# Kernel tuning notes

Measured on AMD Instinct MI355X. Metric: run time of the kernel, lower is better.

## Reference

```python
import jax, jax.numpy as jnp
from jax import lax
import numpy as np

EMBED = 20
FILTERS = 16
KSIZES = (1, 3, 5, 7, 9)
LIN_IN = 7 * len(KSIZES) * FILTERS  # 560
LIN_DIM = 64
SEQ_LENS = {'pep': 12, 'a1': 7, 'a2': 8, 'a3': 16, 'b1': 6, 'b2': 7, 'b3': 18}
BATCH = 16384


def setup_inputs() -> dict:
    key = jax.random.key(0)
    keys = jax.random.split(key, 16)
    inp = {}
    for i, (name, L) in enumerate(SEQ_LENS.items()):
        inp[name] = jax.random.normal(keys[i], (BATCH, EMBED, L), dtype=jnp.float32)
    # Conv weights: one stacked array per kernel size, [7 sequences, FILTERS, EMBED, k]
    for j, k in enumerate(KSIZES):
        inp[f'Wk{k}'] = jax.random.normal(keys[7 + j], (7, FILTERS, EMBED, k), dtype=jnp.float32) * 0.1
    inp['lin1_w'] = jax.random.normal(keys[12], (LIN_DIM, LIN_IN), dtype=jnp.float32) * 0.05
    inp['lin1_b'] = jnp.zeros((LIN_DIM,), dtype=jnp.float32)
    inp['lin2_w'] = jax.random.normal(keys[13], (1, LIN_DIM), dtype=jnp.float32) * 0.1
    inp['lin2_b'] = jnp.zeros((1,), dtype=jnp.float32)
    return inp


def _conv_relu_gmax(x, w):
    # x: [B, C, L], w: [F, C, k] -> SAME conv + ReLU + global max over length -> [B, F]
    y = lax.conv_general_dilated(x, w, window_strides=(1,), padding='SAME',
                                 dimension_numbers=('NCH', 'OIH', 'NCH'))
    return jnp.max(jax.nn.relu(y), axis=-1)


def _branch(x, ws):
    # x scaled by 1/5 as in the torch forward; concat pooled features over kernel sizes
    x = x / 5.0
    return jnp.concatenate([_conv_relu_gmax(x, w) for w in ws], axis=1)  # [B, 5*F]


def reference(pep, a1, a2, a3, b1, b2, b3, Wk1, Wk3, Wk5, Wk7, Wk9,
              lin1_w, lin1_b, lin2_w, lin2_b):
    seqs = [pep, a1, a2, a3, b1, b2, b3]
    Wks = [Wk1, Wk3, Wk5, Wk7, Wk9]
    feats = jnp.concatenate(
        [_branch(seqs[i], [W[i] for W in Wks]) for i in range(7)], axis=1)  # [B, 560]
    # Dropout is identity at inference.
    h = jax.nn.sigmoid(feats @ lin1_w.T + lin1_b)  # [B, 64]
    out = h @ lin2_w.T + lin2_b                    # [B, 1]
    return out.reshape(-1)                          # [B]
```

## Files before the change

kernel.cpp:

```cpp
#include <hip/hip_runtime.h>
#include <stdint.h>
#include <stddef.h>

typedef short bfrag __attribute__((ext_vector_type(8)));
typedef float f32x4 __attribute__((ext_vector_type(4)));

#define NSEQ 7

__constant__ int c_ks[5] = {1, 3, 5, 7, 9};

#define SLO0 3
#define SLO1 2
#define SLO2 1
#define SLO3 0
#define SLO4 0
#define SN0 1
#define SN1 3
#define SN2 5
#define SN3 6
#define SN4 7

static __device__ __forceinline__ unsigned short f2bf(float f) {
  unsigned int u = __float_as_uint(f);
  u += 0x7FFFu + ((u >> 16) & 1u);
  return (unsigned short)(u >> 16);
}

struct PrepArgs {
  const float* Wk[5];
  const float* lin1_w;
  bfrag* Wpack;
  bfrag* lin1pack;
};

__global__ __launch_bounds__(256) void prep_kernel(PrepArgs a) {
  int tid = blockIdx.x * 256 + threadIdx.x;
  const int NW = NSEQ * 5 * 7 * 64;
  if (tid < NW) {
    int lane = tid & 63, rest = tid >> 6;
    int step = rest % 7, nt = (rest / 7) % 5, seq = rest / 35;
    int quad = lane >> 4, f = lane & 15;
    int ks = c_ks[nt], off = (9 - ks) >> 1;
    const float* W = a.Wk[nt];
    bfrag s;
#pragma unroll
    for (int j = 0; j < 8; ++j) {
      int k = step * 32 + quad * 8 + j;
      int t = k / 24, c = k % 24;
      int tap = t - off;
      float val = 0.f;
      if (c < 20 && tap >= 0 && tap < ks)
        val = W[((seq * 16 + f) * 20 + c) * ks + tap] * 0.2f;
      s[j] = (short)f2bf(val);
    }
    a.Wpack[tid] = s;
  } else if (tid < NW + 4 * 18 * 64) {
    int t2 = tid - NW;
    int lane = t2 & 63, rest = t2 >> 6;
    int step = rest % 18, nt = rest / 18;
    int quad = lane >> 4, col = lane & 15;
    int n = nt * 16 + col;
    bfrag s;
#pragma unroll
    for (int j = 0; j < 8; ++j) {
      int k = step * 32 + quad * 8 + j;
      float val = (k < 560) ? a.lin1_w[n * 560 + k] : 0.f;
      s[j] = (short)f2bf(val);
    }
    a.lin1pack[t2] = s;
  }
}

struct ConvArgs {
  const float* x[NSEQ];
  const bfrag* Wpack;
  unsigned short* feats;
};

static __device__ __forceinline__ void store_feat(unsigned short* feats, int b, int k, float v) {
  int step = k >> 5, q = (k >> 3) & 3, j = k & 7;
  feats[((size_t)(b >> 4) * 18 + step) * 512 + (q * 16 + (b & 15)) * 8 + j] = f2bf(v);
}

template <int Lc, int SHIFTc, int MTc, int TBBv, int Pv>
__device__ __forceinline__ void conv_body(unsigned short* xl, const ConvArgs& a,
                                          const int seq, const int b0) {
  const int tid = threadIdx.x;
  const float* xg = a.x[seq];

  for (int i = tid; i < TBBv * Pv * 24 / 8; i += 256) ((uint4*)xl)[i] = uint4{0, 0, 0, 0};
  __syncthreads();
  {
    constexpr int NF4 = TBBv * 20 * Lc / 4;
    const float* xb = xg + (size_t)b0 * 20 * Lc;
    for (int i4 = tid; i4 < NF4; i4 += 256) {
      float4 v = *(const float4*)(xb + i4 * 4);
#pragma unroll
      for (int e = 0; e < 4; ++e) {
        int flat = i4 * 4 + e;
        int b = flat / (20 * Lc), rem = flat % (20 * Lc);
        int c = rem / Lc, xi = rem % Lc;
        float val = (e == 0) ? v.x : (e == 1) ? v.y : (e == 2) ? v.z : v.w;
        xl[(b * Pv + 4 + xi) * 24 + c] = f2bf(val);
      }
    }
  }
  __syncthreads();

  const int wave = tid >> 6, lane = tid & 63, quad = lane >> 4, m = lane & 15;

  const bfrag* wp = a.Wpack + (size_t)(seq * 5 * 7) * 64 + lane;
  bfrag Bf[22];
  {
    int bi = 0;
#pragma unroll
    for (int i = 0; i < SN0; ++i) Bf[bi++] = wp[(0 * 7 + SLO0 + i) * 64];
#pragma unroll
    for (int i = 0; i < SN1; ++i) Bf[bi++] = wp[(1 * 7 + SLO1 + i) * 64];
#pragma unroll
    for (int i = 0; i < SN2; ++i) Bf[bi++] = wp[(2 * 7 + SLO2 + i) * 64];
#pragma unroll
    for (int i = 0; i < SN3; ++i) Bf[bi++] = wp[(3 * 7 + SLO3 + i) * 64];
#pragma unroll
    for (int i = 0; i < SN4; ++i) Bf[bi++] = wp[(4 * 7 + SLO4 + i) * 64];
  }

  constexpr int njobs = (MTc == 2) ? TBBv : ((TBBv << SHIFTc) >> 4);
  constexpr int bpt = (MTc == 1 && SHIFTc == 3) ? 2 : 1;
  constexpr int lmask = (1 << SHIFTc) - 1;

  for (int job = wave; job < njobs; job += 4) {
    float v0 = 0.f, v1 = 0.f, v2 = 0.f, v3 = 0.f, v4 = 0.f;
#pragma unroll
    for (int sub = 0; sub < MTc; ++sub) {
      int bl, l;
      if (MTc == 2) { bl = job; l = sub * 2 + m; }
      else { int r = job * 16 + m; bl = r >> SHIFTc; l = r & lmask; }
      const unsigned short* arow = &xl[(bl * Pv + l) * 24 + quad * 8];
      f32x4 acc0 = {0.f, 0.f, 0.f, 0.f}, acc1 = acc0, acc2 = acc0, acc3 = acc0, acc4 = acc0;
#pragma unroll
      for (int s = 0; s < 7; ++s) {
        bfrag Af = *(const bfrag*)(arow + s * 32);
        if (s >= SLO0 && s < SLO0 + SN0)
          acc0 = __builtin_amdgcn_mfma_f32_16x16x32_bf16(Af, Bf[0 + s - SLO0], acc0, 0, 0, 0);
        if (s >= SLO1 && s < SLO1 + SN1)
          acc1 = __builtin_amdgcn_mfma_f32_16x16x32_bf16(Af, Bf[1 + s - SLO1], acc1, 0, 0, 0);
        if (s >= SLO2 && s < SLO2 + SN2)
          acc2 = __builtin_amdgcn_mfma_f32_16x16x32_bf16(Af, Bf[4 + s - SLO2], acc2, 0, 0, 0);
        if (s >= SLO3 && s < SLO3 + SN3)
          acc3 = __builtin_amdgcn_mfma_f32_16x16x32_bf16(Af, Bf[9 + s - SLO3], acc3, 0, 0, 0);
        acc4 = __builtin_amdgcn_mfma_f32_16x16x32_bf16(Af, Bf[15 + s], acc4, 0, 0, 0);
      }
#pragma unroll
      for (int r4 = 0; r4 < 4; ++r4) {
        bool ok = (MTc == 2) ? true : (((quad * 4 + r4) & lmask) < Lc);
        v0 = fmaxf(v0, ok ? acc0[r4] : 0.f);
        v1 = fmaxf(v1, ok ? acc1[r4] : 0.f);
        v2 = fmaxf(v2, ok ? acc2[r4] : 0.f);
        v3 = fmaxf(v3, ok ? acc3[r4] : 0.f);
        v4 = fmaxf(v4, ok ? acc4[r4] : 0.f);
      }
    }
    v0 = fmaxf(v0, __shfl_xor(v0, 16));
    v1 = fmaxf(v1, __shfl_xor(v1, 16));
    v2 = fmaxf(v2, __shfl_xor(v2, 16));
    v3 = fmaxf(v3, __shfl_xor(v3, 16));
    v4 = fmaxf(v4, __shfl_xor(v4, 16));
    if (bpt == 1) {
      v0 = fmaxf(v0, __shfl_xor(v0, 32));
      v1 = fmaxf(v1, __shfl_xor(v1, 32));
      v2 = fmaxf(v2, __shfl_xor(v2, 32));
      v3 = fmaxf(v3, __shfl_xor(v3, 32));
      v4 = fmaxf(v4, __shfl_xor(v4, 32));
      if (lane < 16) {
        int b = b0 + job, kb = seq * 80 + lane;
        store_feat(a.feats, b, kb, v0);      store_feat(a.feats, b, kb + 16, v1);
        store_feat(a.feats, b, kb + 32, v2); store_feat(a.feats, b, kb + 48, v3);
        store_feat(a.feats, b, kb + 64, v4);
      }
    } else {
      if ((lane & 16) == 0) {
        int b = b0 + job * 2 + (lane >> 5), kb = seq * 80 + (lane & 15);
        store_feat(a.feats, b, kb, v0);      store_feat(a.feats, b, kb + 16, v1);
        store_feat(a.feats, b, kb + 32, v2); store_feat(a.feats, b, kb + 48, v3);
        store_feat(a.feats, b, kb + 64, v4);
      }
    }
  }
}

__global__ __launch_bounds__(256, 4) void conv_kernel(ConvArgs a) {
  __shared__ __align__(16) unsigned short xl[32 * 25 * 24];
  const int bid = blockIdx.x;
  if (bid < 3072) {
    const int seq = bid >> 9, b0 = (bid & 511) * 32;
    switch (seq) {
      case 0: conv_body<12, 4, 1, 32, 25>(xl, a, 0, b0); break;
      case 1: conv_body< 7, 3, 1, 32, 25>(xl, a, 1, b0); break;
      case 2: conv_body< 8, 3, 1, 32, 25>(xl, a, 2, b0); break;
      case 3: conv_body<16, 4, 1, 32, 25>(xl, a, 3, b0); break;
      case 4: conv_body< 6, 3, 1, 32, 25>(xl, a, 4, b0); break;
      default: conv_body< 7, 3, 1, 32, 25>(xl, a, 5, b0); break;
    }
  } else {
    conv_body<18, 5, 2, 16, 41>(xl, a, 6, (bid - 3072) * 16);
  }
}

struct MlpArgs {
  const bfrag* feats;
  const bfrag* lin1pack;
  const float* lin1_b;
  const float* lin2_w;
  const float* lin2_b;
  float* out;
};

__global__ __launch_bounds__(256, 4) void mlp_kernel(MlpArgs a) {
  __shared__ float h[16 * 68];
  __shared__ float w2[64];
  const int tid = threadIdx.x;
  const int b0 = blockIdx.x * 16;
  if (tid < 64) w2[tid] = a.lin2_w[tid];
  const int wave = tid >> 6, lane = tid & 63, quad = lane >> 4, m = lane & 15;
  const int nt = wave;
  bfrag Bf[18];
#pragma unroll
  for (int s = 0; s < 18; ++s) Bf[s] = a.lin1pack[(nt * 18 + s) * 64 + lane];
  const bfrag* ap = a.feats + (size_t)blockIdx.x * 18 * 64 + lane;
  f32x4 acc = {0.f, 0.f, 0.f, 0.f};
#pragma unroll
  for (int s = 0; s < 18; ++s)
    acc = __builtin_amdgcn_mfma_f32_16x16x32_bf16(ap[s * 64], Bf[s], acc, 0, 0, 0);
  int n = nt * 16 + m;
  float bias = a.lin1_b[n];
#pragma unroll
  for (int r = 0; r < 4; ++r) {
    float pre = acc[r] + bias;
    h[(quad * 4 + r) * 68 + n] = 1.f / (1.f + __expf(-pre));
  }
  __syncthreads();
  int bl = tid >> 4, q = tid & 15;
  const float* hr = &h[bl * 68 + q * 4];
  float s = hr[0] * w2[q * 4] + hr[1] * w2[q * 4 + 1] + hr[2] * w2[q * 4 + 2] + hr[3] * w2[q * 4 + 3];
  s += __shfl_xor(s, 1);
  s += __shfl_xor(s, 2);
  s += __shfl_xor(s, 4);
  s += __shfl_xor(s, 8);
  if (q == 0) a.out[b0 + bl] = s + a.lin2_b[0];
}

extern "C" void kernel_launch(void* const* d_in, const int* in_sizes, int n_in,
                              void* d_out, int out_size, void* d_ws, size_t ws_size,
                              hipStream_t stream) {
  (void)in_sizes; (void)n_in; (void)out_size; (void)ws_size;
  char* ws = (char*)d_ws;
  bfrag* Wpack = (bfrag*)(ws + 0);
  bfrag* lin1pack = (bfrag*)(ws + 262144);
  unsigned short* feats = (unsigned short*)(ws + 393216);

  PrepArgs pa;
  for (int j = 0; j < 5; ++j) pa.Wk[j] = (const float*)d_in[7 + j];
  pa.lin1_w = (const float*)d_in[12];
  pa.Wpack = Wpack;
  pa.lin1pack = lin1pack;
  prep_kernel<<<80, 256, 0, stream>>>(pa);

  ConvArgs ca;
  for (int i = 0; i < NSEQ; ++i) ca.x[i] = (const float*)d_in[i];
  ca.Wpack = Wpack;
  ca.feats = feats;
  conv_kernel<<<4096, 256, 0, stream>>>(ca);

  MlpArgs ma;
  ma.feats = (const bfrag*)feats;
  ma.lin1pack = lin1pack;
  ma.lin1_b = (const float*)d_in[13];
  ma.lin2_w = (const float*)d_in[14];
  ma.lin2_b = (const float*)d_in[15];
  ma.out = (float*)d_out;
  mlp_kernel<<<1024, 256, 0, stream>>>(ma);
}
```

Baseline: 188.3 us.

## Process two conv jobs per wave, zero only halos, load rows per thread

New measurement: 198.2 us. 5.2% more time.

```diff
diff --git a/kernel.cpp b/kernel.cpp
--- a/kernel.cpp
+++ b/kernel.cpp
@@ -88,21 +88,26 @@
   const int tid = threadIdx.x;
   const float* xg = a.x[seq];
 
-  for (int i = tid; i < TBBv * Pv * 24 / 8; i += 256) ((uint4*)xl)[i] = uint4{0, 0, 0, 0};
-  __syncthreads();
   {
-    constexpr int NF4 = TBBv * 20 * Lc / 4;
-    const float* xb = xg + (size_t)b0 * 20 * Lc;
-    for (int i4 = tid; i4 < NF4; i4 += 256) {
-      float4 v = *(const float4*)(xb + i4 * 4);
-#pragma unroll
-      for (int e = 0; e < 4; ++e) {
-        int flat = i4 * 4 + e;
-        int b = flat / (20 * Lc), rem = flat % (20 * Lc);
-        int c = rem / Lc, xi = rem % Lc;
-        float val = (e == 0) ? v.x : (e == 1) ? v.y : (e == 2) ? v.z : v.w;
-        xl[(b * Pv + 4 + xi) * 24 + c] = f2bf(val);
-      }
+    constexpr int H1 = 4 * 3;
+    constexpr int H2 = (Pv - 4 - Lc) * 3;
+    uint4* xw = (uint4*)xl;
+    for (int i = tid; i < TBBv * (H1 + H2); i += 256) {
+      int b = i / (H1 + H2), w = i % (H1 + H2);
+      int off = b * Pv * 3 + ((w < H1) ? w : (4 + Lc) * 3 + (w - H1));
+      xw[off] = uint4{0, 0, 0, 0};
+    }
+  }
+  for (int r = tid; r < TBBv * 24; r += 256) {
+    int b = r / 24, c = r % 24;
+    unsigned short* dst = xl + (b * Pv + 4) * 24 + c;
+    if (c < 20) {
+      const float* src = xg + ((size_t)(b0 + b) * 20 + c) * Lc;
+#pragma unroll
+      for (int xi = 0; xi < Lc; ++xi) dst[xi * 24] = f2bf(src[xi]);
+    } else {
+#pragma unroll
+      for (int xi = 0; xi < Lc; ++xi) dst[xi * 24] = 0;
     }
   }
   __syncthreads();
@@ -129,67 +134,83 @@
   constexpr int bpt = (MTc == 1 && SHIFTc == 3) ? 2 : 1;
   constexpr int lmask = (1 << SHIFTc) - 1;
 
-  for (int job = wave; job < njobs; job += 4) {
-    float v0 = 0.f, v1 = 0.f, v2 = 0.f, v3 = 0.f, v4 = 0.f;
+  for (int jj = wave * 2; jj < njobs; jj += 8) {
+    float va[2][5] = {{0.f, 0.f, 0.f, 0.f, 0.f}, {0.f, 0.f, 0.f, 0.f, 0.f}};
 #pragma unroll
     for (int sub = 0; sub < MTc; ++sub) {
-      int bl, l;
-      if (MTc == 2) { bl = job; l = sub * 2 + m; }
-      else { int r = job * 16 + m; bl = r >> SHIFTc; l = r & lmask; }
-      const unsigned short* arow = &xl[(bl * Pv + l) * 24 + quad * 8];
-      f32x4 acc0 = {0.f, 0.f, 0.f, 0.f}, acc1 = acc0, acc2 = acc0, acc3 = acc0, acc4 = acc0;
+      const unsigned short* arow[2];
+#pragma unroll
+      for (int jd = 0; jd < 2; ++jd) {
+        int job = jj + jd, bl, l;
+        if (MTc == 2) { bl = job; l = sub * 2 + m; }
+        else { int rr = job * 16 + m; bl = rr >> SHIFTc; l = rr & lmask; }
+        arow[jd] = &xl[(bl * Pv + l) * 24 + quad * 8];
+      }
+      f32x4 acc[2][5];
+#pragma unroll
+      for (int jd = 0; jd < 2; ++jd)
+#pragma unroll
+        for (int g = 0; g < 5; ++g) acc[jd][g] = f32x4{0.f, 0.f, 0.f, 0.f};
 #pragma unroll
       for (int s = 0; s < 7; ++s) {
-        bfrag Af = *(const bfrag*)(arow + s * 32);
-        if (s >= SLO0 && s < SLO0 + SN0)
-          acc0 = __builtin_amdgcn_mfma_f32_16x16x32_bf16(Af, Bf[0 + s - SLO0], acc0, 0, 0, 0);
-        if (s >= SLO1 && s < SLO1 + SN1)
-          acc1 = __builtin_amdgcn_mfma_f32_16x16x32_bf16(Af, Bf[1 + s - SLO1], acc1, 0, 0, 0);
-        if (s >= SLO2 && s < SLO2 + SN2)
-          acc2 = __builtin_amdgcn_mfma_f32_16x16x32_bf16(Af, Bf[4 + s - SLO2], acc2, 0, 0, 0);
-        if (s >= SLO3 && s < SLO3 + SN3)
-          acc3 = __builtin_amdgcn_mfma_f32_16x16x32_bf16(Af, Bf[9 + s - SLO3], acc3, 0, 0, 0);
-        acc4 = __builtin_amdgcn_mfma_f32_16x16x32_bf16(Af, Bf[15 + s], acc4, 0, 0, 0);
+#pragma unroll
+        for (int jd = 0; jd < 2; ++jd) {
+          bfrag Af = *(const bfrag*)(arow[jd] + s * 32);
+          if (s >= SLO0 && s < SLO0 + SN0)
+            acc[jd][0] = __builtin_amdgcn_mfma_f32_16x16x32_bf16(Af, Bf[0 + s - SLO0], acc[jd][0], 0, 0, 0);
+          if (s >= SLO1 && s < SLO1 + SN1)
+            acc[jd][1] = __builtin_amdgcn_mfma_f32_16x16x32_bf16(Af, Bf[1 + s - SLO1], acc[jd][1], 0, 0, 0);
+          if (s >= SLO2 && s < SLO2 + SN2)
+            acc[jd][2] = __builtin_amdgcn_mfma_f32_16x16x32_bf16(Af, Bf[4 + s - SLO2], acc[jd][2], 0, 0, 0);
+          if (s >= SLO3 && s < SLO3 + SN3)
+            acc[jd][3] = __builtin_amdgcn_mfma_f32_16x16x32_bf16(Af, Bf[9 + s - SLO3], acc[jd][3], 0, 0, 0);
+          acc[jd][4] = __builtin_amdgcn_mfma_f32_16x16x32_bf16(Af, Bf[15 + s], acc[jd][4], 0, 0, 0);
+        }
       }
 #pragma unroll
-      for (int r4 = 0; r4 < 4; ++r4) {
-        bool ok = (MTc == 2) ? true : (((quad * 4 + r4) & lmask) < Lc);
-        v0 = fmaxf(v0, ok ? acc0[r4] : 0.f);
-        v1 = fmaxf(v1, ok ? acc1[r4] : 0.f);
-        v2 = fmaxf(v2, ok ? acc2[r4] : 0.f);
-        v3 = fmaxf(v3, ok ? acc3[r4] : 0.f);
-        v4 = fmaxf(v4, ok ? acc4[r4] : 0.f);
+      for (int jd = 0; jd < 2; ++jd)
+#pragma unroll
+        for (int g = 0; g < 5; ++g)
+#pragma unroll
+          for (int r4 = 0; r4 < 4; ++r4) {
+            bool ok = (MTc == 2) ? true : (((quad * 4 + r4) & lmask) < Lc);
+            va[jd][g] = fmaxf(va[jd][g], ok ? acc[jd][g][r4] : 0.f);
+          }
+    }
+#pragma unroll
+    for (int jd = 0; jd < 2; ++jd) {
+      int job = jj + jd;
+      float v0 = va[jd][0], v1 = va[jd][1], v2 = va[jd][2], v3 = va[jd][3], v4 = va[jd][4];
+      v0 = fmaxf(v0, __shfl_xor(v0, 16));
+      v1 = fmaxf(v1, __shfl_xor(v1, 16));
+      v2 = fmaxf(v2, __shfl_xor(v2, 16));
+      v3 = fmaxf(v3, __shfl_xor(v3, 16));
+      v4 = fmaxf(v4, __shfl_xor(v4, 16));
+      if (bpt == 1) {
+        v0 = fmaxf(v0, __shfl_xor(v0, 32));
+        v1 = fmaxf(v1, __shfl_xor(v1, 32));
+        v2 = fmaxf(v2, __shfl_xor(v2, 32));
+        v3 = fmaxf(v3, __shfl_xor(v3, 32));
+        v4 = fmaxf(v4, __shfl_xor(v4, 32));
+        if (lane < 16) {
+          int b = b0 + job, kb = seq * 80 + lane;
+          store_feat(a.feats, b, kb, v0);      store_feat(a.feats, b, kb + 16, v1);
+          store_feat(a.feats, b, kb + 32, v2); store_feat(a.feats, b, kb + 48, v3);
+          store_feat(a.feats, b, kb + 64, v4);
+        }
+      } else {
+        if ((lane & 16) == 0) {
+          int b = b0 + job * 2 + (lane >> 5), kb = seq * 80 + (lane & 15);
+          store_feat(a.feats, b, kb, v0);      store_feat(a.feats, b, kb + 16, v1);
+          store_feat(a.feats, b, kb + 32, v2); store_feat(a.feats, b, kb + 48, v3);
+          store_feat(a.feats, b, kb + 64, v4);
+        }
       }
     }
-    v0 = fmaxf(v0, __shfl_xor(v0, 16));
-    v1 = fmaxf(v1, __shfl_xor(v1, 16));
-    v2 = fmaxf(v2, __shfl_xor(v2, 16));
-    v3 = fmaxf(v3, __shfl_xor(v3, 16));
-    v4 = fmaxf(v4, __shfl_xor(v4, 16));
-    if (bpt == 1) {
-      v0 = fmaxf(v0, __shfl_xor(v0, 32));
-      v1 = fmaxf(v1, __shfl_xor(v1, 32));
-      v2 = fmaxf(v2, __shfl_xor(v2, 32));
-      v3 = fmaxf(v3, __shfl_xor(v3, 32));
-      v4 = fmaxf(v4, __shfl_xor(v4, 32));
-      if (lane < 16) {
-        int b = b0 + job, kb = seq * 80 + lane;
-        store_feat(a.feats, b, kb, v0);      store_feat(a.feats, b, kb + 16, v1);
-        store_feat(a.feats, b, kb + 32, v2); store_feat(a.feats, b, kb + 48, v3);
-        store_feat(a.feats, b, kb + 64, v4);
-      }
-    } else {
-      if ((lane & 16) == 0) {
-        int b = b0 + job * 2 + (lane >> 5), kb = seq * 80 + (lane & 15);
-        store_feat(a.feats, b, kb, v0);      store_feat(a.feats, b, kb + 16, v1);
-        store_feat(a.feats, b, kb + 32, v2); store_feat(a.feats, b, kb + 48, v3);
-        store_feat(a.feats, b, kb + 64, v4);
-      }
-    }
-  }
-}
-
-__global__ __launch_bounds__(256, 4) void conv_kernel(ConvArgs a) {
+  }
+}
+
+__global__ __launch_bounds__(256, 3) void conv_kernel(ConvArgs a) {
   __shared__ __align__(16) unsigned short xl[32 * 25 * 24];
   const int bid = blockIdx.x;
   if (bid < 3072) {
```
